# Optimization experiments

Measured on AMD Instinct MI355X. Metric: run time of the kernel, lower is better.

Reference implementation:

```python
import jax, jax.numpy as jnp
import numpy as np

DIM = 768
HEADS = 12
HEAD_DIM = DIM // HEADS


def setup_inputs() -> dict:
    key = jax.random.key(0)
    ks = jax.random.split(key, 5)
    B, N = 2, 2048
    x = jax.random.normal(ks[0], (B, N, DIM), dtype=jnp.float32)
    s = 1.0 / np.sqrt(DIM)
    qkv_w = jax.random.normal(ks[1], (3 * DIM, DIM), dtype=jnp.float32) * s
    qkv_b = jnp.zeros((3 * DIM,), dtype=jnp.float32)
    proj_w = jax.random.normal(ks[2], (DIM, DIM), dtype=jnp.float32) * s
    proj_b = jnp.zeros((DIM,), dtype=jnp.float32)
    return {"x": x, "qkv_w": qkv_w, "qkv_b": qkv_b, "proj_w": proj_w, "proj_b": proj_b}


def reference(x, qkv_w, qkv_b, proj_w, proj_b):
    B, N, C = x.shape
    scale = HEAD_DIM ** -0.5
    qkv = x @ qkv_w.T + qkv_b                      # [B,N,3C]
    qkv = qkv.reshape(B, N, 3, HEADS, HEAD_DIM)
    q = qkv[:, :, 0].transpose(0, 2, 1, 3)         # [B,H,N,D]
    k = qkv[:, :, 1].transpose(0, 2, 1, 3)
    v = qkv[:, :, 2].transpose(0, 2, 1, 3)
    attn = jnp.einsum('bhnd,bhmd->bhnm', q, k) * scale
    attn = jax.nn.softmax(attn, axis=-1)
    out = jnp.einsum('bhnm,bhmd->bhnd', attn, v)   # [B,H,N,D]
    out = out.transpose(0, 2, 1, 3).reshape(B, N, C)
    return out @ proj_w.T + proj_b
```

## Files before the change

### kernel.cpp

```cpp
#include <hip/hip_runtime.h>
#include <hip/hip_bf16.h>

typedef __bf16 bf16x8 __attribute__((ext_vector_type(8)));
typedef float f32x4 __attribute__((ext_vector_type(4)));
typedef float f32x16 __attribute__((ext_vector_type(16)));

#define SEQ   2048
#define NHEAD 12
#define NBH   24
#define QSCALE 0.18033688011112042f

#define CP16(g, l) __builtin_amdgcn_global_load_lds( \
    (const __attribute__((address_space(1))) unsigned int*)(g), \
    (__attribute__((address_space(3))) unsigned int*)(l), 16, 0, 0)

__device__ __forceinline__ unsigned short f2bf(float f) {
  unsigned int u = __builtin_bit_cast(unsigned int, f);
  u += 0x7FFFu + ((u >> 16) & 1u);
  return (unsigned short)(u >> 16);
}
__device__ __forceinline__ unsigned int packbf2_trunc(float lo, float hi) {
  return __builtin_amdgcn_perm(__builtin_bit_cast(unsigned int, hi),
                               __builtin_bit_cast(unsigned int, lo), 0x07060302u);
}

#define NX4  786432
#define NW14 442368
__global__ __launch_bounds__(256) void cvt3_kernel(const float4* __restrict__ x,
                                                   const float4* __restrict__ w1,
                                                   const float4* __restrict__ w2,
                                                   ushort4* __restrict__ xo,
                                                   ushort4* __restrict__ w1o,
                                                   ushort4* __restrict__ w2o) {
  int i = blockIdx.x * 256 + threadIdx.x;
  const float4* s;
  ushort4* d;
  int j = i;
  if (i < NX4)               { s = x;  d = xo; }
  else if (i < NX4 + NW14)   { s = w1; d = w1o; j = i - NX4; }
  else                       { s = w2; d = w2o; j = i - (NX4 + NW14); }
  float4 v = s[j];
  ushort4 r;
  r.x = f2bf(v.x); r.y = f2bf(v.y); r.z = f2bf(v.z); r.w = f2bf(v.w);
  d[j] = r;
}

template <int BM, int BN, int MODE>
__global__ __launch_bounds__(256) void gemm_kernel(const unsigned short* __restrict__ X,
                                                   const unsigned short* __restrict__ W,
                                                   const float* __restrict__ bias,
                                                   unsigned short* __restrict__ Qb,
                                                   unsigned short* __restrict__ Kb,
                                                   unsigned short* __restrict__ Vtb,
                                                   float* __restrict__ Out) {
  constexpr int K = 768, BK = 64;
  constexpr int WM = BM / 2, WN = BN / 2;
  constexpr int MT = WM / 16, NT = WN / 16;
  __shared__ __align__(16) unsigned short Xs[BM * BK];
  __shared__ __align__(16) unsigned short Ws[BN * BK];

  const int tid = threadIdx.x;
  const int w = tid >> 6, lane = tid & 63, quad = lane >> 4, m16 = lane & 15;
  const int wm = w & 1, wn = w >> 1;
  const int row0 = blockIdx.y * BM, col0 = blockIdx.x * BN;

  f32x4 acc[MT][NT];
#pragma unroll
  for (int mt = 0; mt < MT; ++mt)
#pragma unroll
    for (int nt = 0; nt < NT; ++nt) acc[mt][nt] = (f32x4){0.f, 0.f, 0.f, 0.f};

  for (int k0 = 0; k0 < K; k0 += BK) {
    __syncthreads();
#pragma unroll
    for (int j = 0; j < BM / 32; ++j) {
      int e = tid + 256 * j, r = e >> 3, c8 = e & 7;
      CP16(X + (size_t)(row0 + r) * 768 + k0 + ((c8 ^ (r & 7)) << 3), Xs + e * 8);
    }
#pragma unroll
    for (int j = 0; j < BN / 32; ++j) {
      int e = tid + 256 * j, r = e >> 3, c8 = e & 7;
      CP16(W + (size_t)(col0 + r) * 768 + k0 + ((c8 ^ (r & 7)) << 3), Ws + e * 8);
    }
    __syncthreads();
#pragma unroll
    for (int ks = 0; ks < 2; ++ks) {
      const int sw = ((quad + 4 * ks) ^ (m16 & 7)) << 3;
      bf16x8 a[MT], b[NT];
#pragma unroll
      for (int mt = 0; mt < MT; ++mt)
        a[mt] = *(const bf16x8*)(Xs + (wm * WM + mt * 16 + m16) * BK + sw);
#pragma unroll
      for (int nt = 0; nt < NT; ++nt)
        b[nt] = *(const bf16x8*)(Ws + (wn * WN + nt * 16 + m16) * BK + sw);
#pragma unroll
      for (int mt = 0; mt < MT; ++mt)
#pragma unroll
        for (int nt = 0; nt < NT; ++nt)
          acc[mt][nt] = __builtin_amdgcn_mfma_f32_16x16x32_bf16(a[mt], b[nt], acc[mt][nt], 0, 0, 0);
    }
  }

#pragma unroll
  for (int mt = 0; mt < MT; ++mt) {
#pragma unroll
    for (int nt = 0; nt < NT; ++nt) {
      const int m0 = row0 + wm * WM + mt * 16 + quad * 4;
      const int c = col0 + wn * WN + nt * 16 + m16;
      const float bia = bias[c];
      f32x4 v = acc[mt][nt];
      if constexpr (MODE == 0) {
        const int bidx = m0 >> 11, ns = m0 & 2047;
        if (c < 1536) {
          unsigned short* dst;
          float sc;
          int cc;
          if (c < 768) { cc = c; dst = Qb; sc = QSCALE; }
          else         { cc = c - 768; dst = Kb; sc = 1.0f; }
          const int h = cc >> 6, d = cc & 63;
          unsigned short* p = dst + ((size_t)(bidx * NHEAD + h) * SEQ + ns) * 64 + d;
          p[0]   = f2bf((v[0] + bia) * sc);
          p[64]  = f2bf((v[1] + bia) * sc);
          p[128] = f2bf((v[2] + bia) * sc);
          p[192] = f2bf((v[3] + bia) * sc);
        } else {
          const int cc = c - 1536, h = cc >> 6, d = cc & 63;
          const int ns2 = (ns & ~12) | ((ns & 4) << 1) | ((ns & 8) >> 1);
          ushort4 pk;
          pk.x = f2bf(v[0] + bia); pk.y = f2bf(v[1] + bia);
          pk.z = f2bf(v[2] + bia); pk.w = f2bf(v[3] + bia);
          *(ushort4*)(Vtb + ((size_t)(bidx * NHEAD + h) * 64 + d) * SEQ + ns2) = pk;
        }
      } else {
        float* o = Out + (size_t)m0 * 768 + c;
        o[0]       = v[0] + bia;
        o[768]     = v[1] + bia;
        o[2 * 768] = v[2] + bia;
        o[3 * 768] = v[3] + bia;
      }
    }
  }
}

__global__ __launch_bounds__(128) void attn_kernel(const unsigned short* __restrict__ Qb,
                                                   const unsigned short* __restrict__ Kb,
                                                   const unsigned short* __restrict__ Vtb,
                                                   unsigned short* __restrict__ Ab) {
  __shared__ __align__(16) unsigned short Ks[2][64 * 64];
  __shared__ __align__(16) unsigned short Vts[2][64 * 64];

  const int tid = threadIdx.x;
  const int w = tid >> 6, lane = tid & 63, hi = lane >> 5, l32 = lane & 31;
  const int bh = blockIdx.x % NBH, qt = blockIdx.x / NBH;
  const int bb = bh / NHEAD, h = bh % NHEAD;
  const int q0 = qt * 64 + w * 32;

  const unsigned short* Qp = Qb + (size_t)bh * SEQ * 64;
  const unsigned short* Kp = Kb + (size_t)bh * SEQ * 64;
  const unsigned short* Vp = Vtb + (size_t)bh * 64 * SEQ;

  bf16x8 qf[4];
#pragma unroll
  for (int dc = 0; dc < 4; ++dc)
    qf[dc] = *(const bf16x8*)(Qp + (size_t)(q0 + l32) * 64 + dc * 16 + hi * 8);

#pragma unroll
  for (int j = 0; j < 4; ++j) {
    int e = tid + 128 * j, r = e >> 3, c8 = e & 7;
    CP16(Kp + (size_t)r * 64 + ((c8 ^ (r & 7)) << 3), &Ks[0][e * 8]);
    CP16(Vp + (size_t)r * SEQ + ((c8 ^ (r & 7)) << 3), &Vts[0][e * 8]);
  }

  f32x16 o[2] = {};
  float m_i = -3.0e38f, l_i = 0.f;

  for (int kt = 0; kt < 32; ++kt) {
    const int cur = kt & 1;
    __syncthreads();

    const unsigned short* Kc = Ks[cur];
    const unsigned short* Vc = Vts[cur];
    bf16x8 kf[2][4], vf[2][4];
#pragma unroll
    for (int t32 = 0; t32 < 2; ++t32)
#pragma unroll
      for (int dc = 0; dc < 4; ++dc)
        kf[t32][dc] = *(const bf16x8*)(Kc + (t32 * 32 + l32) * 64 + ((((dc << 1) | hi) ^ (l32 & 7)) << 3));
#pragma unroll
    for (int dt = 0; dt < 2; ++dt)
#pragma unroll
      for (int cc = 0; cc < 4; ++cc)
        vf[dt][cc] = *(const bf16x8*)(Vc + (dt * 32 + l32) * 64 + ((((cc << 1) | hi) ^ (l32 & 7)) << 3));

    if (kt < 31) {
      const int kn = kt + 1, nb = 1 - cur;
#pragma unroll
      for (int j = 0; j < 4; ++j) {
        int e = tid + 128 * j, r = e >> 3, c8 = e & 7;
        CP16(Kp + (size_t)(kn * 64 + r) * 64 + ((c8 ^ (r & 7)) << 3), &Ks[nb][e * 8]);
        CP16(Vp + (size_t)r * SEQ + kn * 64 + ((c8 ^ (r & 7)) << 3), &Vts[nb][e * 8]);
      }
    }

    f32x16 st[2];
#pragma unroll
    for (int t32 = 0; t32 < 2; ++t32) {
      f32x16 s = {};
#pragma unroll
      for (int dc = 0; dc < 4; ++dc)
        s = __builtin_amdgcn_mfma_f32_32x32x16_bf16(kf[t32][dc], qf[dc], s, 0, 0, 0);
      st[t32] = s;
    }

    float tmax = st[0][0];
#pragma unroll
    for (int t32 = 0; t32 < 2; ++t32)
#pragma unroll
      for (int e = 0; e < 16; ++e) tmax = fmaxf(tmax, st[t32][e]);
    tmax = fmaxf(tmax, __shfl_xor(tmax, 32));
    const float mnew = fmaxf(m_i, tmax);
    const float alpha = __builtin_amdgcn_exp2f(m_i - mnew);
    float ssum = 0.f;
    unsigned int pf[2][8];
#pragma unroll
    for (int t32 = 0; t32 < 2; ++t32) {
      float pv[16];
#pragma unroll
      for (int e = 0; e < 16; ++e) { pv[e] = __builtin_amdgcn_exp2f(st[t32][e] - mnew); ssum += pv[e]; }
#pragma unroll
      for (int e2 = 0; e2 < 8; ++e2)
        pf[t32][e2] = packbf2_trunc(pv[2 * e2], pv[2 * e2 + 1]);
    }
    ssum += __shfl_xor(ssum, 32);
    l_i = l_i * alpha + ssum;
    m_i = mnew;
    o[0] *= alpha;
    o[1] *= alpha;

#pragma unroll
    for (int t32 = 0; t32 < 2; ++t32) {
#pragma unroll
      for (int hh = 0; hh < 2; ++hh) {
        bf16x8 pfrag = __builtin_bit_cast(bf16x8,
            make_uint4(pf[t32][hh * 4], pf[t32][hh * 4 + 1], pf[t32][hh * 4 + 2], pf[t32][hh * 4 + 3]));
        const int cc = 2 * t32 + hh;
#pragma unroll
        for (int dt = 0; dt < 2; ++dt)
          o[dt] = __builtin_amdgcn_mfma_f32_32x32x16_bf16(vf[dt][cc], pfrag, o[dt], 0, 0, 0);
      }
    }
  }

  const float rl = __builtin_amdgcn_rcpf(l_i);
  unsigned short* base = Ab + ((size_t)bb * SEQ + q0 + l32) * 768 + h * 64;
#pragma unroll
  for (int dt = 0; dt < 2; ++dt) {
#pragma unroll
    for (int run = 0; run < 4; ++run) {
      ushort4 pk;
      pk.x = f2bf(o[dt][run * 4 + 0] * rl);
      pk.y = f2bf(o[dt][run * 4 + 1] * rl);
      pk.z = f2bf(o[dt][run * 4 + 2] * rl);
      pk.w = f2bf(o[dt][run * 4 + 3] * rl);
      *(ushort4*)(base + dt * 32 + run * 8 + hi * 4) = pk;
    }
  }
}

extern "C" void kernel_launch(void* const* d_in, const int* in_sizes, int n_in,
                              void* d_out, int out_size, void* d_ws, size_t ws_size,
                              hipStream_t stream) {
  const float* x      = (const float*)d_in[0];
  const float* qkv_w  = (const float*)d_in[1];
  const float* qkv_b  = (const float*)d_in[2];
  const float* proj_w = (const float*)d_in[3];
  const float* proj_b = (const float*)d_in[4];
  float* out = (float*)d_out;

  unsigned short* xb  = (unsigned short*)d_ws;
  unsigned short* wqb = xb + 3145728;
  unsigned short* wpb = wqb + 1769472;
  unsigned short* Qb  = wpb + 589824;
  unsigned short* Kb  = Qb + 3145728;
  unsigned short* Vtb = Kb + 3145728;
  unsigned short* Ab  = Vtb + 3145728;

  cvt3_kernel<<<5376, 256, 0, stream>>>((const float4*)x, (const float4*)qkv_w, (const float4*)proj_w,
                                        (ushort4*)xb, (ushort4*)wqb, (ushort4*)wpb);
  gemm_kernel<128, 96, 0><<<dim3(24, 32), 256, 0, stream>>>(xb, wqb, qkv_b, Qb, Kb, Vtb, nullptr);
  attn_kernel<<<768, 128, 0, stream>>>(Qb, Kb, Vtb, Ab);
  gemm_kernel<64, 96, 1><<<dim3(8, 64), 256, 0, stream>>>(Ab, wpb, proj_b, nullptr, nullptr, nullptr, out);
}
```

Baseline: 169.5 us.

## Deepen attention K/V pipeline with register-prefetched K fragments and setprio

```diff
diff --git a/kernel.cpp b/kernel.cpp
--- a/kernel.cpp
+++ b/kernel.cpp
@@ -22,6 +22,13 @@
 __device__ __forceinline__ unsigned int packbf2_trunc(float lo, float hi) {
   return __builtin_amdgcn_perm(__builtin_bit_cast(unsigned int, hi),
                                __builtin_bit_cast(unsigned int, lo), 0x07060302u);
+}
+__device__ __forceinline__ float vmax16(const f32x16& s) {
+  float a = fmaxf(fmaxf(s[0], s[1]), fmaxf(s[2], s[3]));
+  float b = fmaxf(fmaxf(s[4], s[5]), fmaxf(s[6], s[7]));
+  float c = fmaxf(fmaxf(s[8], s[9]), fmaxf(s[10], s[11]));
+  float d = fmaxf(fmaxf(s[12], s[13]), fmaxf(s[14], s[15]));
+  return fmaxf(fmaxf(a, b), fmaxf(c, d));
 }
 
 #define NX4  786432
@@ -142,12 +149,11 @@
   }
 }
 
-__global__ __launch_bounds__(128) void attn_kernel(const unsigned short* __restrict__ Qb,
-                                                   const unsigned short* __restrict__ Kb,
-                                                   const unsigned short* __restrict__ Vtb,
-                                                   unsigned short* __restrict__ Ab) {
-  __shared__ __align__(16) unsigned short Ks[2][64 * 64];
-  __shared__ __align__(16) unsigned short Vts[2][64 * 64];
+__global__ __launch_bounds__(128, 1) void attn_kernel(const unsigned short* __restrict__ Qb,
+                                                      const unsigned short* __restrict__ Kb,
+                                                      const unsigned short* __restrict__ Vtb,
+                                                      unsigned short* __restrict__ Ab) {
+  __shared__ __align__(16) unsigned short S[24576];
 
   const int tid = threadIdx.x;
   const int w = tid >> 6, lane = tid & 63, hi = lane >> 5, l32 = lane & 31;
@@ -164,94 +170,117 @@
   for (int dc = 0; dc < 4; ++dc)
     qf[dc] = *(const bf16x8*)(Qp + (size_t)(q0 + l32) * 64 + dc * 16 + hi * 8);
 
+  const unsigned short* dsK[2][4];
+  const unsigned short* dsV[2][4];
+#pragma unroll
+  for (int t32 = 0; t32 < 2; ++t32)
+#pragma unroll
+    for (int c = 0; c < 4; ++c) {
+      dsK[t32][c] = &S[(t32 * 32 + l32) * 64 + ((((c << 1) | hi) ^ (l32 & 7)) << 3)];
+      dsV[t32][c] = dsK[t32][c] + 16384;
+    }
+
+  const unsigned short* Kst[4];
+  const unsigned short* Vst[4];
 #pragma unroll
   for (int j = 0; j < 4; ++j) {
-    int e = tid + 128 * j, r = e >> 3, c8 = e & 7;
-    CP16(Kp + (size_t)r * 64 + ((c8 ^ (r & 7)) << 3), &Ks[0][e * 8]);
-    CP16(Vp + (size_t)r * SEQ + ((c8 ^ (r & 7)) << 3), &Vts[0][e * 8]);
-  }
+    const int e = tid + 128 * j, r = e >> 3, sw = ((e & 7) ^ (r & 7)) << 3;
+    Kst[j] = Kp + r * 64 + sw;
+    Vst[j] = Vp + r * SEQ + sw;
+  }
+  const int edst = tid * 8;
+
+#pragma unroll
+  for (int j = 0; j < 4; ++j) {
+    CP16(Kst[j], &S[edst + 1024 * j]);
+    CP16(Vst[j], &S[16384 + edst + 1024 * j]);
+  }
+  __syncthreads();
+  bf16x8 kfA[2][4], kfB[2][4];
+#pragma unroll
+  for (int t32 = 0; t32 < 2; ++t32)
+#pragma unroll
+    for (int c = 0; c < 4; ++c)
+      kfA[t32][c] = *(const bf16x8*)(dsK[t32][c]);
+#pragma unroll
+  for (int j = 0; j < 4; ++j)
+    CP16(Kst[j] + 4096, &S[4096 + edst + 1024 * j]);
 
   f32x16 o[2] = {};
-  float m_i = -3.0e38f, l_i = 0.f;
-
-  for (int kt = 0; kt < 32; ++kt) {
-    const int cur = kt & 1;
-    __syncthreads();
-
-    const unsigned short* Kc = Ks[cur];
-    const unsigned short* Vc = Vts[cur];
-    bf16x8 kf[2][4], vf[2][4];
-#pragma unroll
-    for (int t32 = 0; t32 < 2; ++t32)
-#pragma unroll
-      for (int dc = 0; dc < 4; ++dc)
-        kf[t32][dc] = *(const bf16x8*)(Kc + (t32 * 32 + l32) * 64 + ((((dc << 1) | hi) ^ (l32 & 7)) << 3));
-#pragma unroll
-    for (int dt = 0; dt < 2; ++dt)
-#pragma unroll
-      for (int cc = 0; cc < 4; ++cc)
-        vf[dt][cc] = *(const bf16x8*)(Vc + (dt * 32 + l32) * 64 + ((((cc << 1) | hi) ^ (l32 & 7)) << 3));
-
-    if (kt < 31) {
-      const int kn = kt + 1, nb = 1 - cur;
-#pragma unroll
-      for (int j = 0; j < 4; ++j) {
-        int e = tid + 128 * j, r = e >> 3, c8 = e & 7;
-        CP16(Kp + (size_t)(kn * 64 + r) * 64 + ((c8 ^ (r & 7)) << 3), &Ks[nb][e * 8]);
-        CP16(Vp + (size_t)r * SEQ + kn * 64 + ((c8 ^ (r & 7)) << 3), &Vts[nb][e * 8]);
-      }
-    }
-
-    f32x16 st[2];
-#pragma unroll
-    for (int t32 = 0; t32 < 2; ++t32) {
-      f32x16 s = {};
-#pragma unroll
-      for (int dc = 0; dc < 4; ++dc)
-        s = __builtin_amdgcn_mfma_f32_32x32x16_bf16(kf[t32][dc], qf[dc], s, 0, 0, 0);
-      st[t32] = s;
-    }
-
-    float tmax = st[0][0];
-#pragma unroll
-    for (int t32 = 0; t32 < 2; ++t32)
-#pragma unroll
-      for (int e = 0; e < 16; ++e) tmax = fmaxf(tmax, st[t32][e]);
-    tmax = fmaxf(tmax, __shfl_xor(tmax, 32));
-    const float mnew = fmaxf(m_i, tmax);
-    const float alpha = __builtin_amdgcn_exp2f(m_i - mnew);
-    float ssum = 0.f;
-    unsigned int pf[2][8];
-#pragma unroll
-    for (int t32 = 0; t32 < 2; ++t32) {
-      float pv[16];
-#pragma unroll
-      for (int e = 0; e < 16; ++e) { pv[e] = __builtin_amdgcn_exp2f(st[t32][e] - mnew); ssum += pv[e]; }
-#pragma unroll
-      for (int e2 = 0; e2 < 8; ++e2)
-        pf[t32][e2] = packbf2_trunc(pv[2 * e2], pv[2 * e2 + 1]);
-    }
-    ssum += __shfl_xor(ssum, 32);
-    l_i = l_i * alpha + ssum;
-    m_i = mnew;
-    o[0] *= alpha;
-    o[1] *= alpha;
-
-#pragma unroll
-    for (int t32 = 0; t32 < 2; ++t32) {
-#pragma unroll
-      for (int hh = 0; hh < 2; ++hh) {
-        bf16x8 pfrag = __builtin_bit_cast(bf16x8,
-            make_uint4(pf[t32][hh * 4], pf[t32][hh * 4 + 1], pf[t32][hh * 4 + 2], pf[t32][hh * 4 + 3]));
-        const int cc = 2 * t32 + hh;
-#pragma unroll
-        for (int dt = 0; dt < 2; ++dt)
-          o[dt] = __builtin_amdgcn_mfma_f32_32x32x16_bf16(vf[dt][cc], pfrag, o[dt], 0, 0, 0);
-      }
-    }
-  }
-
-  const float rl = __builtin_amdgcn_rcpf(l_i);
+  f32x16 lacc = {};
+  float m_i = -3.0e38f;
+
+#define TILE_STEP(J, KC, KN)                                                              \
+  {                                                                                       \
+    __syncthreads();                      \
+    _Pragma("unroll") for (int t32 = 0; t32 < 2; ++t32)                                   \
+      _Pragma("unroll") for (int c = 0; c < 4; ++c)                                       \
+        KN[t32][c] = *(const bf16x8*)(dsK[t32][c] + (((J) + 1) & 3) * 4096);              \
+    bf16x8 vf[2][4];                                                                      \
+    _Pragma("unroll") for (int dt = 0; dt < 2; ++dt)                                      \
+      _Pragma("unroll") for (int c = 0; c < 4; ++c)                                       \
+        vf[dt][c] = *(const bf16x8*)(dsV[dt][c] + ((J) & 1) * 4096);                      \
+    _Pragma("unroll") for (int jj = 0; jj < 4; ++jj) {                                    \
+      CP16(Kst[jj] + kt4 * 16384 + ((J) + 2) * 4096,                                      \
+           &S[(((J) + 2) & 3) * 4096 + edst + 1024 * jj]);                                \
+      CP16(Vst[jj] + kt4 * 256 + ((J) + 1) * 64,                                          \
+           &S[16384 + (((J) + 1) & 1) * 4096 + edst + 1024 * jj]);                        \
+    }                                                                                     \
+    __builtin_amdgcn_s_setprio(1);                                                        \
+    f32x16 st[2];                                                                         \
+    _Pragma("unroll") for (int t32 = 0; t32 < 2; ++t32) {                                 \
+      f32x16 s = {};                                                                      \
+      _Pragma("unroll") for (int dc = 0; dc < 4; ++dc)                                    \
+        s = __builtin_amdgcn_mfma_f32_32x32x16_bf16(KC[t32][dc], qf[dc], s, 0, 0, 0);     \
+      st[t32] = s;                                                                        \
+    }                                                                                     \
+    __builtin_amdgcn_s_setprio(0);                                                        \
+    float tmax = fmaxf(vmax16(st[0]), vmax16(st[1]));                                     \
+    tmax = fmaxf(tmax, __shfl_xor(tmax, 32));                                             \
+    const float mnew = fmaxf(m_i, tmax);                                                  \
+    const float alpha = __builtin_amdgcn_exp2f(m_i - mnew);                               \
+    m_i = mnew;                                                                           \
+    o[0] *= alpha;                                                                        \
+    o[1] *= alpha;                                                                        \
+    lacc *= alpha;                                                                        \
+    unsigned int pf[2][8];                                                                \
+    _Pragma("unroll") for (int t32 = 0; t32 < 2; ++t32) {                                 \
+      float pv[16];                                                                       \
+      _Pragma("unroll") for (int e = 0; e < 16; ++e)                                      \
+        pv[e] = __builtin_amdgcn_exp2f(st[t32][e] - mnew);                                \
+      _Pragma("unroll") for (int e = 0; e < 16; ++e) lacc[e] += pv[e];                    \
+      _Pragma("unroll") for (int e2 = 0; e2 < 8; ++e2)                                    \
+        pf[t32][e2] = packbf2_trunc(pv[2 * e2], pv[2 * e2 + 1]);                          \
+    }                                                                                     \
+    __builtin_amdgcn_s_setprio(1);                                                        \
+    _Pragma("unroll") for (int t32 = 0; t32 < 2; ++t32)                                   \
+      _Pragma("unroll") for (int hh = 0; hh < 2; ++hh) {                                  \
+        bf16x8 pfrag = __builtin_bit_cast(bf16x8,                                         \
+            make_uint4(pf[t32][hh * 4], pf[t32][hh * 4 + 1],                              \
+                       pf[t32][hh * 4 + 2], pf[t32][hh * 4 + 3]));                        \
+        _Pragma("unroll") for (int dt = 0; dt < 2; ++dt)                                  \
+          o[dt] = __builtin_amdgcn_mfma_f32_32x32x16_bf16(vf[dt][2 * t32 + hh], pfrag,    \
+                                                          o[dt], 0, 0, 0);                \
+      }                                                                                   \
+    __builtin_amdgcn_s_setprio(0);                                                        \
+  }
+
+  for (int kt4 = 0; kt4 < 8; ++kt4) {
+    TILE_STEP(0, kfA, kfB)
+    TILE_STEP(1, kfB, kfA)
+    TILE_STEP(2, kfA, kfB)
+    TILE_STEP(3, kfB, kfA)
+  }
+#undef TILE_STEP
+
+  float l4[4];
+#pragma unroll
+  for (int g = 0; g < 4; ++g)
+    l4[g] = (lacc[4 * g] + lacc[4 * g + 1]) + (lacc[4 * g + 2] + lacc[4 * g + 3]);
+  float lsum = (l4[0] + l4[1]) + (l4[2] + l4[3]);
+  lsum += __shfl_xor(lsum, 32);
+  const float rl = __builtin_amdgcn_rcpf(lsum);
+
   unsigned short* base = Ab + ((size_t)bb * SEQ + q0 + l32) * 768 + h * 64;
 #pragma unroll
   for (int dt = 0; dt < 2; ++dt) {
```

New measurement: 186.3 us. +9.9%, slower.

## Double-buffer LDS tiles in projection GEMM to overlap loads with MFMA

Applied to the files above, without the earlier changes.

```diff
diff --git a/kernel.cpp b/kernel.cpp
--- a/kernel.cpp
+++ b/kernel.cpp
@@ -53,11 +53,11 @@
                                                    unsigned short* __restrict__ Kb,
                                                    unsigned short* __restrict__ Vtb,
                                                    float* __restrict__ Out) {
-  constexpr int K = 768, BK = 64;
+  constexpr int K = 768, BK = 64, NKT = K / BK;
   constexpr int WM = BM / 2, WN = BN / 2;
   constexpr int MT = WM / 16, NT = WN / 16;
-  __shared__ __align__(16) unsigned short Xs[BM * BK];
-  __shared__ __align__(16) unsigned short Ws[BN * BK];
+  __shared__ __align__(16) unsigned short Xs[2][BM * BK];
+  __shared__ __align__(16) unsigned short Ws[2][BN * BK];
 
   const int tid = threadIdx.x;
   const int w = tid >> 6, lane = tid & 63, quad = lane >> 4, m16 = lane & 15;
@@ -70,35 +70,55 @@
 #pragma unroll
     for (int nt = 0; nt < NT; ++nt) acc[mt][nt] = (f32x4){0.f, 0.f, 0.f, 0.f};
 
-  for (int k0 = 0; k0 < K; k0 += BK) {
+#pragma unroll
+  for (int j = 0; j < BM / 32; ++j) {
+    int e = tid + 256 * j, r = e >> 3, c8 = e & 7;
+    CP16(X + (size_t)(row0 + r) * 768 + ((c8 ^ (r & 7)) << 3), &Xs[0][e * 8]);
+  }
+#pragma unroll
+  for (int j = 0; j < BN / 32; ++j) {
+    int e = tid + 256 * j, r = e >> 3, c8 = e & 7;
+    CP16(W + (size_t)(col0 + r) * 768 + ((c8 ^ (r & 7)) << 3), &Ws[0][e * 8]);
+  }
+
+#pragma unroll 2
+  for (int kt = 0; kt < NKT; ++kt) {
+    const int cur = kt & 1;
     __syncthreads();
-#pragma unroll
-    for (int j = 0; j < BM / 32; ++j) {
-      int e = tid + 256 * j, r = e >> 3, c8 = e & 7;
-      CP16(X + (size_t)(row0 + r) * 768 + k0 + ((c8 ^ (r & 7)) << 3), Xs + e * 8);
-    }
-#pragma unroll
-    for (int j = 0; j < BN / 32; ++j) {
-      int e = tid + 256 * j, r = e >> 3, c8 = e & 7;
-      CP16(W + (size_t)(col0 + r) * 768 + k0 + ((c8 ^ (r & 7)) << 3), Ws + e * 8);
-    }
-    __syncthreads();
+
+    bf16x8 a[2][MT], b[2][NT];
 #pragma unroll
     for (int ks = 0; ks < 2; ++ks) {
       const int sw = ((quad + 4 * ks) ^ (m16 & 7)) << 3;
-      bf16x8 a[MT], b[NT];
 #pragma unroll
       for (int mt = 0; mt < MT; ++mt)
-        a[mt] = *(const bf16x8*)(Xs + (wm * WM + mt * 16 + m16) * BK + sw);
+        a[ks][mt] = *(const bf16x8*)(&Xs[cur][(wm * WM + mt * 16 + m16) * BK + sw]);
 #pragma unroll
       for (int nt = 0; nt < NT; ++nt)
-        b[nt] = *(const bf16x8*)(Ws + (wn * WN + nt * 16 + m16) * BK + sw);
+        b[ks][nt] = *(const bf16x8*)(&Ws[cur][(wn * WN + nt * 16 + m16) * BK + sw]);
+    }
+
+    if (kt < NKT - 1) {
+      const int k0n = (kt + 1) * BK, nb = 1 - cur;
+#pragma unroll
+      for (int j = 0; j < BM / 32; ++j) {
+        int e = tid + 256 * j, r = e >> 3, c8 = e & 7;
+        CP16(X + (size_t)(row0 + r) * 768 + k0n + ((c8 ^ (r & 7)) << 3), &Xs[nb][e * 8]);
+      }
+#pragma unroll
+      for (int j = 0; j < BN / 32; ++j) {
+        int e = tid + 256 * j, r = e >> 3, c8 = e & 7;
+        CP16(W + (size_t)(col0 + r) * 768 + k0n + ((c8 ^ (r & 7)) << 3), &Ws[nb][e * 8]);
+      }
+    }
+
+#pragma unroll
+    for (int ks = 0; ks < 2; ++ks)
 #pragma unroll
       for (int mt = 0; mt < MT; ++mt)
 #pragma unroll
         for (int nt = 0; nt < NT; ++nt)
-          acc[mt][nt] = __builtin_amdgcn_mfma_f32_16x16x32_bf16(a[mt], b[nt], acc[mt][nt], 0, 0, 0);
-    }
+          acc[mt][nt] = __builtin_amdgcn_mfma_f32_16x16x32_bf16(a[ks][mt], b[ks][nt], acc[mt][nt], 0, 0, 0);
   }
 
 #pragma unroll
```

Result: no change. 168.9 us (-0.3%).
